# Kernel optimization log

Hardware: AMD Instinct MI355X
Metric: run time of the kernel (lower is better)

Reference implementation:

```python
import jax, jax.numpy as jnp
import numpy as np

B, S, T = 4, 4096, 2048
SD, TD, H = 512, 768, 8
D = SD // H
EPS = 1e-5
ALPHA_MAX = 0.5


def layer_norm(x, g, b):
    mu = jnp.mean(x, axis=-1, keepdims=True)
    var = jnp.mean(jnp.square(x - mu), axis=-1, keepdims=True)
    return (x - mu) * jax.lax.rsqrt(var + EPS) * g + b


def setup_inputs() -> dict:
    key = jax.random.key(0)
    ks = jax.random.split(key, 12)
    inp = {
        "source": jax.random.normal(ks[0], (B, S, SD), jnp.float32),
        "target": jax.random.normal(ks[1], (B, T, TD), jnp.float32),
        "target_mask": jax.random.randint(ks[2], (B, T), 0, 2, jnp.int32),
        # layer norms
        "ns_g": jnp.ones((SD,), jnp.float32), "ns_b": jnp.zeros((SD,), jnp.float32),
        "nt_g": jnp.ones((TD,), jnp.float32), "nt_b": jnp.zeros((TD,), jnp.float32),
        "no_g": jnp.ones((SD,), jnp.float32), "no_b": jnp.zeros((SD,), jnp.float32),
        # projections, stored (in, out); xavier-uniform with gains as in _init_weights
        "Wq": jax.random.uniform(ks[3], (SD, SD), jnp.float32, -1, 1) * (0.5 * np.sqrt(6.0 / (SD + SD))),
        "bq": jnp.zeros((SD,), jnp.float32),
        "Wk": jax.random.uniform(ks[4], (TD, SD), jnp.float32, -1, 1) * (0.5 * np.sqrt(6.0 / (TD + SD))),
        "bk": jnp.zeros((SD,), jnp.float32),
        "Wv": jax.random.uniform(ks[5], (TD, SD), jnp.float32, -1, 1) * (0.5 * np.sqrt(6.0 / (TD + SD))),
        "bv": jnp.zeros((SD,), jnp.float32),
        "Wo": jax.random.uniform(ks[6], (SD, SD), jnp.float32, -1, 1) * (0.25 * np.sqrt(6.0 / (SD + SD))),
        "bo": jnp.zeros((SD,), jnp.float32),
        "alpha_raw": jnp.asarray(0.1, jnp.float32),
    }
    return inp


def reference(source, target, target_mask, ns_g, ns_b, nt_g, nt_b, no_g, no_b,
              Wq, bq, Wk, bk, Wv, bv, Wo, bo, alpha_raw):
    scale = D ** -0.5
    src_n = layer_norm(source, ns_g, ns_b)
    tgt_n = layer_norm(target, nt_g, nt_b)
    Q = (src_n @ Wq + bq).reshape(B, S, H, D)
    K = (tgt_n @ Wk + bk).reshape(B, T, H, D)
    V = (tgt_n @ Wv + bv).reshape(B, T, H, D)
    attn = jnp.einsum('bshd,bthd->bhst', Q, K) * scale
    attn = jnp.clip(attn, -50.0, 50.0)
    mask = (target_mask == 0)[:, None, None, :]  # (B,1,1,T)
    attn = jnp.where(mask, -jnp.inf, attn)
    attn = jax.nn.softmax(attn, axis=-1)
    attn = jnp.nan_to_num(attn, nan=0.0)
    out = jnp.einsum('bhst,bthd->bshd', attn, V).reshape(B, S, SD)
    out = out @ Wo + bo
    out = layer_norm(out, no_g, no_b)
    alpha = ALPHA_MAX * (jnp.tanh(alpha_raw) + 1.0) / 2.0
    return source + alpha * out
```

## Files before the change

### kernel.cpp

```cpp
#include <hip/hip_runtime.h>
#include <math.h>

#define BB 4
#define SS 4096
#define TT 2048
#define SDIM 512
#define TDIM 768
#define NH 8
#define HD 64

typedef __attribute__((ext_vector_type(8))) short s8v;
typedef __attribute__((ext_vector_type(4))) short s4v;
typedef __attribute__((ext_vector_type(4))) float f32x4;
typedef __attribute__((ext_vector_type(4))) unsigned int u32x4;

__device__ inline unsigned short f2bf(float f) {
    unsigned int u = __float_as_uint(f);
    u += 0x7FFFu + ((u >> 16) & 1u);
    return (unsigned short)(u >> 16);
}

__device__ inline unsigned int cvtpk_bf16(float lo, float hi) {
    unsigned int r;
    asm("v_cvt_pk_bf16_f32 %0, %1, %2" : "=v"(r) : "v"(lo), "v"(hi));
    return r;
}

__global__ __launch_bounds__(256) void prep_w(const float* __restrict__ W,
                                              unsigned short* __restrict__ Wt,
                                              int K, int N, float scale) {
    __shared__ float tile[32][33];
    const int n0 = blockIdx.x * 32, k0 = blockIdx.y * 32;
    const int tx = threadIdx.x & 31, ty = threadIdx.x >> 5;
#pragma unroll
    for (int i = 0; i < 4; ++i) {
        const int k = ty + i * 8;
        tile[k][tx] = W[(size_t)(k0 + k) * N + n0 + tx];
    }
    __syncthreads();
#pragma unroll
    for (int i = 0; i < 4; ++i) {
        const int n = ty + i * 8;
        Wt[(size_t)(n0 + n) * K + k0 + tx] = f2bf(tile[tx][n] * scale);
    }
}

template <int W, int BLK>
__global__ __launch_bounds__(BLK) void ln_rows_bf(const float* __restrict__ x,
                                                  const float* __restrict__ g,
                                                  const float* __restrict__ bb,
                                                  unsigned short* __restrict__ y) {
    const int row = blockIdx.x;
    const int t = threadIdx.x;
    float4 v = *(const float4*)(x + (size_t)row * W + t * 4);
    float s = v.x + v.y + v.z + v.w;
    float q = v.x * v.x + v.y * v.y + v.z * v.z + v.w * v.w;
#pragma unroll
    for (int off = 32; off > 0; off >>= 1) {
        s += __shfl_down(s, off, 64);
        q += __shfl_down(q, off, 64);
    }
    constexpr int NW = BLK / 64;
    __shared__ float redS[NW], redQ[NW];
    if ((t & 63) == 0) { redS[t >> 6] = s; redQ[t >> 6] = q; }
    __syncthreads();
    float S = 0.f, Q = 0.f;
#pragma unroll
    for (int i = 0; i < NW; ++i) { S += redS[i]; Q += redQ[i]; }
    const float mu = S * (1.0f / W);
    const float var = Q * (1.0f / W) - mu * mu;
    const float rstd = rsqrtf(var + 1e-5f);
    const float4 gv = *(const float4*)(g + t * 4);
    const float4 bv = *(const float4*)(bb + t * 4);
    s4v o;
    o[0] = (short)f2bf((v.x - mu) * rstd * gv.x + bv.x);
    o[1] = (short)f2bf((v.y - mu) * rstd * gv.y + bv.y);
    o[2] = (short)f2bf((v.z - mu) * rstd * gv.z + bv.z);
    o[3] = (short)f2bf((v.w - mu) * rstd * gv.w + bv.w);
    *(s4v*)(y + (size_t)row * W + t * 4) = o;
}

__global__ __launch_bounds__(128) void ln_res(const float* __restrict__ x,
                                              const float* __restrict__ src,
                                              const float* __restrict__ g,
                                              const float* __restrict__ bb,
                                              const float* __restrict__ alpha_raw,
                                              float* __restrict__ out) {
    const int W = 512;
    const int row = blockIdx.x;
    const int t = threadIdx.x;
    float4 v = *(const float4*)(x + (size_t)row * W + t * 4);
    float s = v.x + v.y + v.z + v.w;
    float q = v.x * v.x + v.y * v.y + v.z * v.z + v.w * v.w;
#pragma unroll
    for (int off = 32; off > 0; off >>= 1) {
        s += __shfl_down(s, off, 64);
        q += __shfl_down(q, off, 64);
    }
    __shared__ float redS[2], redQ[2];
    if ((t & 63) == 0) { redS[t >> 6] = s; redQ[t >> 6] = q; }
    __syncthreads();
    const float S = redS[0] + redS[1];
    const float Q = redQ[0] + redQ[1];
    const float mu = S * (1.0f / W);
    const float var = Q * (1.0f / W) - mu * mu;
    const float rstd = rsqrtf(var + 1e-5f);
    const float alpha = 0.25f * (tanhf(alpha_raw[0]) + 1.0f);
    const float4 gv = *(const float4*)(g + t * 4);
    const float4 bv = *(const float4*)(bb + t * 4);
    const float4 sv = *(const float4*)(src + (size_t)row * W + t * 4);
    float4 o;
    o.x = sv.x + alpha * ((v.x - mu) * rstd * gv.x + bv.x);
    o.y = sv.y + alpha * ((v.y - mu) * rstd * gv.y + bv.y);
    o.z = sv.z + alpha * ((v.z - mu) * rstd * gv.z + bv.z);
    o.w = sv.w + alpha * ((v.w - mu) * rstd * gv.w + bv.w);
    *(float4*)(out + (size_t)row * W + t * 4) = o;
}

template <int OUT>
__global__ __launch_bounds__(256) void gemm_mfma(const unsigned short* __restrict__ A,
                                                 const unsigned short* __restrict__ Bt,
                                                 const float* __restrict__ bias,
                                                 void* __restrict__ C,
                                                 int N, int K, float bscale) {
    __shared__ __align__(16) char A_lds[128 * 128];
    __shared__ __align__(16) char B_lds[128 * 128];
    const int tid = threadIdx.x;
    const int l = tid & 63;
    const int lq = l & 15, q = l >> 4;
    const int w = tid >> 6;
    const int wr = w >> 1, wc = w & 1;
    const int m0 = blockIdx.y * 128, n0 = blockIdx.x * 128;

    f32x4 acc[4][4];
#pragma unroll
    for (int i = 0; i < 4; ++i)
#pragma unroll
        for (int j = 0; j < 4; ++j) acc[i][j] = (f32x4){0.f, 0.f, 0.f, 0.f};

    const int sr = tid >> 1;
    const int sc = (tid & 1) * 64;
    const int swz = (sr & 7) << 4;

    for (int k0 = 0; k0 < K; k0 += 64) {
        const unsigned short* ap = A + (size_t)(m0 + sr) * K + k0 + (sc >> 1);
        const unsigned short* bp = Bt + (size_t)(n0 + sr) * K + k0 + (sc >> 1);
#pragma unroll
        for (int c = 0; c < 4; ++c) {
            const s8v av = *(const s8v*)(ap + c * 8);
            *(s8v*)(A_lds + sr * 128 + ((sc + c * 16) ^ swz)) = av;
        }
#pragma unroll
        for (int c = 0; c < 4; ++c) {
            const s8v bv = *(const s8v*)(bp + c * 8);
            *(s8v*)(B_lds + sr * 128 + ((sc + c * 16) ^ swz)) = bv;
        }
        __syncthreads();
#pragma unroll
        for (int db = 0; db < 2; ++db) {
            s8v af[4], bf[4];
#pragma unroll
            for (int i = 0; i < 4; ++i) {
                const int ra = wr * 64 + i * 16 + lq;
                af[i] = *(const s8v*)(A_lds + ra * 128 + ((db * 64 + q * 16) ^ ((ra & 7) << 4)));
                const int rb = wc * 64 + i * 16 + lq;
                bf[i] = *(const s8v*)(B_lds + rb * 128 + ((db * 64 + q * 16) ^ ((rb & 7) << 4)));
            }
#pragma unroll
            for (int i = 0; i < 4; ++i)
#pragma unroll
                for (int j = 0; j < 4; ++j)
                    acc[i][j] = __builtin_amdgcn_mfma_f32_16x16x32_bf16(af[i], bf[j], acc[i][j], 0, 0, 0);
        }
        __syncthreads();
    }
#pragma unroll
    for (int i = 0; i < 4; ++i) {
#pragma unroll
        for (int j = 0; j < 4; ++j) {
            const int col = n0 + wc * 64 + j * 16 + lq;
            const float bs = bias[col] * bscale;
            const int mr0 = m0 + wr * 64 + i * 16 + q * 4;
            if (OUT == 0) {
                unsigned short* Cp = (unsigned short*)C;
#pragma unroll
                for (int r = 0; r < 4; ++r)
                    Cp[(size_t)(mr0 + r) * N + col] = f2bf(acc[i][j][r] + bs);
            } else if (OUT == 1) {
                float* Cp = (float*)C;
#pragma unroll
                for (int r = 0; r < 4; ++r)
                    Cp[(size_t)(mr0 + r) * N + col] = acc[i][j][r] + bs;
            } else {
                s4v o4;
#pragma unroll
                for (int r = 0; r < 4; ++r) o4[r] = (short)f2bf(acc[i][j][r] + bs);
                unsigned short* Cp = (unsigned short*)C;
                *(s4v*)(Cp + ((size_t)((mr0 >> 11) * SDIM + col)) * TT + (mr0 & 2047)) = o4;
            }
        }
    }
}

__global__ __launch_bounds__(256) void attn_mfma(const unsigned short* __restrict__ Qg,
                                                 const unsigned short* __restrict__ Kg,
                                                 const unsigned short* __restrict__ Vt,
                                                 const int* __restrict__ mask,
                                                 unsigned short* __restrict__ O) {
    __shared__ __align__(16) char K_lds[64 * 128];
    __shared__ __align__(16) char V_lds[64 * 128];
    __shared__ __align__(16) float Msb[64];
    const int b = blockIdx.y >> 3, h = blockIdx.y & 7;
    const int tid = threadIdx.x;
    const int w = tid >> 6, l = tid & 63;
    const int lq = l & 15, q = l >> 4;
    const int qrow = blockIdx.x * 64 + w * 16 + lq;

    s8v qf[2];
    {
        const unsigned short* qp = Qg + ((size_t)b * SS + qrow) * SDIM + h * HD + q * 8;
        qf[0] = *(const s8v*)(qp);
        qf[1] = *(const s8v*)(qp + 32);
    }
    f32x4 accO[4];
#pragma unroll
    for (int i = 0; i < 4; ++i) accO[i] = (f32x4){0.f, 0.f, 0.f, 0.f};
    float lsum = 0.f;

    const int sr = tid >> 2;
    const int sc = (tid & 3) * 32;
    const int swz = (sr & 7) << 4;

    for (int t0 = 0; t0 < TT; t0 += 64) {
        {
            const unsigned short* kp = Kg + ((size_t)b * TT + t0 + sr) * SDIM + h * HD + (sc >> 1);
            const s8v k0 = *(const s8v*)kp;
            const s8v k1 = *(const s8v*)(kp + 8);
            *(s8v*)(K_lds + sr * 128 + (sc ^ swz)) = k0;
            *(s8v*)(K_lds + sr * 128 + ((sc + 16) ^ swz)) = k1;
            const unsigned short* vp = Vt + ((size_t)(b * SDIM + h * HD + sr)) * TT + t0 + (sc >> 1);
            const s8v v0 = *(const s8v*)vp;
            const s8v v1 = *(const s8v*)(vp + 8);
            *(s8v*)(V_lds + sr * 128 + (sc ^ swz)) = v0;
            *(s8v*)(V_lds + sr * 128 + ((sc + 16) ^ swz)) = v1;
            if (tid < 64) Msb[tid] = (mask[b * TT + t0 + tid] == 0) ? -1e30f : 0.f;
        }
        __syncthreads();

        f32x4 accS[4];
#pragma unroll
        for (int kt = 0; kt < 4; ++kt) accS[kt] = *(const f32x4*)(Msb + kt * 16 + q * 4);
#pragma unroll
        for (int kt = 0; kt < 4; ++kt) {
            const int row = kt * 16 + lq;
            const int rs = (row & 7) << 4;
#pragma unroll
            for (int db = 0; db < 2; ++db) {
                const s8v af = *(const s8v*)(K_lds + row * 128 + ((db * 64 + q * 16) ^ rs));
                accS[kt] = __builtin_amdgcn_mfma_f32_16x16x32_bf16(af, qf[db], accS[kt], 0, 0, 0);
            }
        }
        float p[4][4];
#pragma unroll
        for (int kt = 0; kt < 4; ++kt) {
#pragma unroll
            for (int r = 0; r < 4; ++r) {
                const float pv = __expf(accS[kt][r]);
                p[kt][r] = pv;
                lsum += pv;
            }
        }
#pragma unroll
        for (int kb = 0; kb < 2; ++kb) {
            const int a = kb * 2;
            u32x4 pw;
            pw[0] = cvtpk_bf16(p[a][0], p[a][1]);
            pw[1] = cvtpk_bf16(p[a][2], p[a][3]);
            pw[2] = cvtpk_bf16(p[a + 1][0], p[a + 1][1]);
            pw[3] = cvtpk_bf16(p[a + 1][2], p[a + 1][3]);
            const s8v pb = __builtin_bit_cast(s8v, pw);
#pragma unroll
            for (int nt = 0; nt < 4; ++nt) {
                const int row = nt * 16 + lq;
                const int rs = (row & 7) << 4;
                const s4v lo = *(const s4v*)(V_lds + row * 128 + ((kb * 64 + q * 8) ^ rs));
                const s4v hi = *(const s4v*)(V_lds + row * 128 + ((kb * 64 + 32 + q * 8) ^ rs));
                const s8v vf = __builtin_shufflevector(lo, hi, 0, 1, 2, 3, 4, 5, 6, 7);
                accO[nt] = __builtin_amdgcn_mfma_f32_16x16x32_bf16(vf, pb, accO[nt], 0, 0, 0);
            }
        }
        __syncthreads();
    }
    lsum += __shfl_xor(lsum, 16, 64);
    lsum += __shfl_xor(lsum, 32, 64);
    const float inv = (lsum > 0.f) ? 1.0f / lsum : 0.f;
    unsigned short* op = O + ((size_t)b * SS + qrow) * SDIM + h * HD + q * 4;
#pragma unroll
    for (int nt = 0; nt < 4; ++nt) {
        s4v o4;
#pragma unroll
        for (int r = 0; r < 4; ++r) o4[r] = (short)f2bf(accO[nt][r] * inv);
        *(s4v*)(op + nt * 16) = o4;
    }
}

extern "C" void kernel_launch(void* const* d_in, const int* in_sizes, int n_in,
                              void* d_out, int out_size, void* d_ws, size_t ws_size,
                              hipStream_t stream) {
    const float* src = (const float*)d_in[0];
    const float* tgt = (const float*)d_in[1];
    const int* tmask = (const int*)d_in[2];
    const float* ns_g = (const float*)d_in[3];
    const float* ns_b = (const float*)d_in[4];
    const float* nt_g = (const float*)d_in[5];
    const float* nt_b = (const float*)d_in[6];
    const float* no_g = (const float*)d_in[7];
    const float* no_b = (const float*)d_in[8];
    const float* Wq = (const float*)d_in[9];
    const float* bq = (const float*)d_in[10];
    const float* Wk = (const float*)d_in[11];
    const float* bk = (const float*)d_in[12];
    const float* Wv = (const float*)d_in[13];
    const float* bv = (const float*)d_in[14];
    const float* Wo = (const float*)d_in[15];
    const float* bo = (const float*)d_in[16];
    const float* alpha_raw = (const float*)d_in[17];

    char* ws = (char*)d_ws;
    unsigned short* src_n = (unsigned short*)ws; ws += (size_t)16384 * 512 * 2;
    unsigned short* tgt_n = (unsigned short*)ws; ws += (size_t)8192 * 768 * 2;
    unsigned short* Qb    = (unsigned short*)ws; ws += (size_t)16384 * 512 * 2;
    unsigned short* Kb    = (unsigned short*)ws; ws += (size_t)8192 * 512 * 2;
    unsigned short* Vtb   = (unsigned short*)ws; ws += (size_t)8192 * 512 * 2;
    unsigned short* Oa    = (unsigned short*)ws; ws += (size_t)16384 * 512 * 2;
    float*          Opj   = (float*)ws;          ws += (size_t)16384 * 512 * 4;
    unsigned short* Wtq   = (unsigned short*)ws; ws += (size_t)512 * 512 * 2;
    unsigned short* Wtk   = (unsigned short*)ws; ws += (size_t)512 * 768 * 2;
    unsigned short* Wtv   = (unsigned short*)ws; ws += (size_t)512 * 768 * 2;
    unsigned short* Wto   = (unsigned short*)ws; ws += (size_t)512 * 512 * 2;

    prep_w<<<dim3(16, 16), 256, 0, stream>>>(Wq, Wtq, 512, 512, 0.125f);
    prep_w<<<dim3(16, 24), 256, 0, stream>>>(Wk, Wtk, 768, 512, 1.0f);
    prep_w<<<dim3(16, 24), 256, 0, stream>>>(Wv, Wtv, 768, 512, 1.0f);
    prep_w<<<dim3(16, 16), 256, 0, stream>>>(Wo, Wto, 512, 512, 1.0f);

    ln_rows_bf<512, 128><<<16384, 128, 0, stream>>>(src, ns_g, ns_b, src_n);
    ln_rows_bf<768, 192><<<8192, 192, 0, stream>>>(tgt, nt_g, nt_b, tgt_n);

    gemm_mfma<0><<<dim3(4, 128), 256, 0, stream>>>(src_n, Wtq, bq, Qb, 512, 512, 0.125f);
    gemm_mfma<0><<<dim3(4, 64), 256, 0, stream>>>(tgt_n, Wtk, bk, Kb, 512, 768, 1.0f);
    gemm_mfma<2><<<dim3(4, 64), 256, 0, stream>>>(tgt_n, Wtv, bv, Vtb, 512, 768, 1.0f);

    attn_mfma<<<dim3(64, 32), 256, 0, stream>>>(Qb, Kb, Vtb, tmask, Oa);

    gemm_mfma<1><<<dim3(4, 128), 256, 0, stream>>>(Oa, Wto, bo, Opj, 512, 512, 1.0f);

    ln_res<<<16384, 128, 0, stream>>>(Opj, src, no_g, no_b, alpha_raw, (float*)d_out);
}
```

Measured before the change: 368.0 us.

## Double-buffer attention K/V tiles, widen query block, shrink GEMM N-tile, merge weight prep

The attention kernel now double-buffers K, V and mask tiles in LDS, prefetching the next tile into registers while computing the current one. Each wave handles two 16-row query groups so every K/V fragment read from LDS feeds two MFMAs, and MFMA sections are bracketed with s_setprio. The projection GEMMs use a 128x64 tile instead of 128x128, doubling grid size for better CU occupancy and wave count. The four weight-prep launches are merged into one 3D-grid launch. Costs are doubled LDS for attention, extra registers for the prefetch and the second query group, and more B-tile reloads in the GEMMs.

```diff
diff --git a/kernel.cpp b/kernel.cpp
--- a/kernel.cpp
+++ b/kernel.cpp
@@ -26,11 +26,24 @@
     return r;
 }
 
-__global__ __launch_bounds__(256) void prep_w(const float* __restrict__ W,
-                                              unsigned short* __restrict__ Wt,
-                                              int K, int N, float scale) {
+__global__ __launch_bounds__(256) void prep_w4(const float* __restrict__ W0,
+                                               const float* __restrict__ W1,
+                                               const float* __restrict__ W2,
+                                               const float* __restrict__ W3,
+                                               unsigned short* __restrict__ T0,
+                                               unsigned short* __restrict__ T1,
+                                               unsigned short* __restrict__ T2,
+                                               unsigned short* __restrict__ T3) {
+    const int z = blockIdx.z;
+    const int K = (z == 1 || z == 2) ? 768 : 512;
+    const int k0 = blockIdx.y * 32;
+    if (k0 >= K) return;
+    const float* W = (z == 0) ? W0 : (z == 1) ? W1 : (z == 2) ? W2 : W3;
+    unsigned short* Wt = (z == 0) ? T0 : (z == 1) ? T1 : (z == 2) ? T2 : T3;
+    const float scale = (z == 0) ? 0.125f : 1.0f;
+    const int N = 512;
     __shared__ float tile[32][33];
-    const int n0 = blockIdx.x * 32, k0 = blockIdx.y * 32;
+    const int n0 = blockIdx.x * 32;
     const int tx = threadIdx.x & 31, ty = threadIdx.x >> 5;
 #pragma unroll
     for (int i = 0; i < 4; ++i) {
@@ -124,52 +137,58 @@
                                                  void* __restrict__ C,
                                                  int N, int K, float bscale) {
     __shared__ __align__(16) char A_lds[128 * 128];
-    __shared__ __align__(16) char B_lds[128 * 128];
+    __shared__ __align__(16) char B_lds[64 * 128];
     const int tid = threadIdx.x;
     const int l = tid & 63;
     const int lq = l & 15, q = l >> 4;
     const int w = tid >> 6;
     const int wr = w >> 1, wc = w & 1;
-    const int m0 = blockIdx.y * 128, n0 = blockIdx.x * 128;
-
-    f32x4 acc[4][4];
+    const int m0 = blockIdx.y * 128, n0 = blockIdx.x * 64;
+
+    f32x4 acc[4][2];
 #pragma unroll
     for (int i = 0; i < 4; ++i)
 #pragma unroll
-        for (int j = 0; j < 4; ++j) acc[i][j] = (f32x4){0.f, 0.f, 0.f, 0.f};
+        for (int j = 0; j < 2; ++j) acc[i][j] = (f32x4){0.f, 0.f, 0.f, 0.f};
 
     const int sr = tid >> 1;
     const int sc = (tid & 1) * 64;
-    const int swz = (sr & 7) << 4;
+    const int swzA = (sr & 7) << 4;
+    const int sr2 = tid >> 2;
+    const int sc2 = (tid & 3) * 32;
+    const int swzB = (sr2 & 7) << 4;
 
     for (int k0 = 0; k0 < K; k0 += 64) {
         const unsigned short* ap = A + (size_t)(m0 + sr) * K + k0 + (sc >> 1);
-        const unsigned short* bp = Bt + (size_t)(n0 + sr) * K + k0 + (sc >> 1);
+        const unsigned short* bp = Bt + (size_t)(n0 + sr2) * K + k0 + (sc2 >> 1);
 #pragma unroll
         for (int c = 0; c < 4; ++c) {
             const s8v av = *(const s8v*)(ap + c * 8);
-            *(s8v*)(A_lds + sr * 128 + ((sc + c * 16) ^ swz)) = av;
-        }
-#pragma unroll
-        for (int c = 0; c < 4; ++c) {
+            *(s8v*)(A_lds + sr * 128 + ((sc + c * 16) ^ swzA)) = av;
+        }
+#pragma unroll
+        for (int c = 0; c < 2; ++c) {
             const s8v bv = *(const s8v*)(bp + c * 8);
-            *(s8v*)(B_lds + sr * 128 + ((sc + c * 16) ^ swz)) = bv;
+            *(s8v*)(B_lds + sr2 * 128 + ((sc2 + c * 16) ^ swzB)) = bv;
         }
         __syncthreads();
 #pragma unroll
         for (int db = 0; db < 2; ++db) {
-            s8v af[4], bf[4];
+            s8v af[4], bf[2];
 #pragma unroll
             for (int i = 0; i < 4; ++i) {
                 const int ra = wr * 64 + i * 16 + lq;
                 af[i] = *(const s8v*)(A_lds + ra * 128 + ((db * 64 + q * 16) ^ ((ra & 7) << 4)));
-                const int rb = wc * 64 + i * 16 + lq;
-                bf[i] = *(const s8v*)(B_lds + rb * 128 + ((db * 64 + q * 16) ^ ((rb & 7) << 4)));
+            }
+#pragma unroll
+            for (int j = 0; j < 2; ++j) {
+                const int rb = wc * 32 + j * 16 + lq;
+                bf[j] = *(const s8v*)(B_lds + rb * 128 + ((db * 64 + q * 16) ^ ((rb & 7) << 4)));
             }
 #pragma unroll
             for (int i = 0; i < 4; ++i)
 #pragma unroll
-                for (int j = 0; j < 4; ++j)
+                for (int j = 0; j < 2; ++j)
                     acc[i][j] = __builtin_amdgcn_mfma_f32_16x16x32_bf16(af[i], bf[j], acc[i][j], 0, 0, 0);
         }
         __syncthreads();
@@ -177,8 +196,8 @@
 #pragma unroll
     for (int i = 0; i < 4; ++i) {
 #pragma unroll
-        for (int j = 0; j < 4; ++j) {
-            const int col = n0 + wc * 64 + j * 16 + lq;
+        for (int j = 0; j < 2; ++j) {
+            const int col = n0 + wc * 32 + j * 16 + lq;
             const float bs = bias[col] * bscale;
             const int mr0 = m0 + wr * 64 + i * 16 + q * 4;
             if (OUT == 0) {
@@ -207,100 +226,136 @@
                                                  const unsigned short* __restrict__ Vt,
                                                  const int* __restrict__ mask,
                                                  unsigned short* __restrict__ O) {
-    __shared__ __align__(16) char K_lds[64 * 128];
-    __shared__ __align__(16) char V_lds[64 * 128];
-    __shared__ __align__(16) float Msb[64];
+    __shared__ __align__(16) char K_lds[2][64 * 128];
+    __shared__ __align__(16) char V_lds[2][64 * 128];
+    __shared__ __align__(16) float Msb[2][64];
     const int b = blockIdx.y >> 3, h = blockIdx.y & 7;
     const int tid = threadIdx.x;
     const int w = tid >> 6, l = tid & 63;
     const int lq = l & 15, q = l >> 4;
-    const int qrow = blockIdx.x * 64 + w * 16 + lq;
-
-    s8v qf[2];
+    const int qbase = blockIdx.x * 128 + w * 32;
+
+    s8v qf[2][2];
+#pragma unroll
+    for (int qa = 0; qa < 2; ++qa) {
+        const unsigned short* qp = Qg + ((size_t)b * SS + qbase + qa * 16 + lq) * SDIM + h * HD + q * 8;
+        qf[qa][0] = *(const s8v*)(qp);
+        qf[qa][1] = *(const s8v*)(qp + 32);
+    }
+    f32x4 accO[2][4];
+#pragma unroll
+    for (int qa = 0; qa < 2; ++qa)
+#pragma unroll
+        for (int nt = 0; nt < 4; ++nt) accO[qa][nt] = (f32x4){0.f, 0.f, 0.f, 0.f};
+    float lsum[2] = {0.f, 0.f};
+
+    const int sr = tid >> 2;
+    const int scb = (tid & 3) * 32;
+    const int swz = (sr & 7) << 4;
+    const unsigned short* kp_base = Kg + ((size_t)b * TT + sr) * SDIM + h * HD + (scb >> 1);
+    const unsigned short* vp_base = Vt + ((size_t)(b * SDIM + h * HD + sr)) * TT + (scb >> 1);
+
     {
-        const unsigned short* qp = Qg + ((size_t)b * SS + qrow) * SDIM + h * HD + q * 8;
-        qf[0] = *(const s8v*)(qp);
-        qf[1] = *(const s8v*)(qp + 32);
-    }
-    f32x4 accO[4];
-#pragma unroll
-    for (int i = 0; i < 4; ++i) accO[i] = (f32x4){0.f, 0.f, 0.f, 0.f};
-    float lsum = 0.f;
-
-    const int sr = tid >> 2;
-    const int sc = (tid & 3) * 32;
-    const int swz = (sr & 7) << 4;
+        const s8v k0r = *(const s8v*)kp_base;
+        const s8v k1r = *(const s8v*)(kp_base + 8);
+        const s8v v0r = *(const s8v*)vp_base;
+        const s8v v1r = *(const s8v*)(vp_base + 8);
+        *(s8v*)(K_lds[0] + sr * 128 + (scb ^ swz)) = k0r;
+        *(s8v*)(K_lds[0] + sr * 128 + ((scb + 16) ^ swz)) = k1r;
+        *(s8v*)(V_lds[0] + sr * 128 + (scb ^ swz)) = v0r;
+        *(s8v*)(V_lds[0] + sr * 128 + ((scb + 16) ^ swz)) = v1r;
+        if (tid < 64) Msb[0][tid] = (mask[b * TT + tid] == 0) ? -1e30f : 0.f;
+    }
+    __syncthreads();
 
     for (int t0 = 0; t0 < TT; t0 += 64) {
-        {
-            const unsigned short* kp = Kg + ((size_t)b * TT + t0 + sr) * SDIM + h * HD + (sc >> 1);
-            const s8v k0 = *(const s8v*)kp;
-            const s8v k1 = *(const s8v*)(kp + 8);
-            *(s8v*)(K_lds + sr * 128 + (sc ^ swz)) = k0;
-            *(s8v*)(K_lds + sr * 128 + ((sc + 16) ^ swz)) = k1;
-            const unsigned short* vp = Vt + ((size_t)(b * SDIM + h * HD + sr)) * TT + t0 + (sc >> 1);
-            const s8v v0 = *(const s8v*)vp;
-            const s8v v1 = *(const s8v*)(vp + 8);
-            *(s8v*)(V_lds + sr * 128 + (sc ^ swz)) = v0;
-            *(s8v*)(V_lds + sr * 128 + ((sc + 16) ^ swz)) = v1;
-            if (tid < 64) Msb[tid] = (mask[b * TT + t0 + tid] == 0) ? -1e30f : 0.f;
-        }
-        __syncthreads();
-
-        f32x4 accS[4];
-#pragma unroll
-        for (int kt = 0; kt < 4; ++kt) accS[kt] = *(const f32x4*)(Msb + kt * 16 + q * 4);
+        const int cur = (t0 >> 6) & 1, nxt = cur ^ 1;
+        const bool has_next = (t0 + 64) < TT;
+
+        s8v kn0, kn1, vn0, vn1;
+        int mn = 0;
+        if (has_next) {
+            const unsigned short* kp = kp_base + (size_t)(t0 + 64) * SDIM;
+            const unsigned short* vp = vp_base + (t0 + 64);
+            kn0 = *(const s8v*)kp;
+            kn1 = *(const s8v*)(kp + 8);
+            vn0 = *(const s8v*)vp;
+            vn1 = *(const s8v*)(vp + 8);
+            if (tid < 64) mn = mask[b * TT + t0 + 64 + tid];
+        }
+
+        u32x4 pb[2][2];
 #pragma unroll
         for (int kt = 0; kt < 4; ++kt) {
             const int row = kt * 16 + lq;
             const int rs = (row & 7) << 4;
+            const f32x4 mb = *(const f32x4*)(&Msb[cur][kt * 16 + q * 4]);
+            f32x4 aS0 = mb, aS1 = mb;
+            __builtin_amdgcn_s_setprio(1);
 #pragma unroll
             for (int db = 0; db < 2; ++db) {
-                const s8v af = *(const s8v*)(K_lds + row * 128 + ((db * 64 + q * 16) ^ rs));
-                accS[kt] = __builtin_amdgcn_mfma_f32_16x16x32_bf16(af, qf[db], accS[kt], 0, 0, 0);
-            }
-        }
-        float p[4][4];
-#pragma unroll
-        for (int kt = 0; kt < 4; ++kt) {
-#pragma unroll
-            for (int r = 0; r < 4; ++r) {
-                const float pv = __expf(accS[kt][r]);
-                p[kt][r] = pv;
-                lsum += pv;
+                const s8v af = *(const s8v*)(K_lds[cur] + row * 128 + ((db * 64 + q * 16) ^ rs));
+                aS0 = __builtin_amdgcn_mfma_f32_16x16x32_bf16(af, qf[0][db], aS0, 0, 0, 0);
+                aS1 = __builtin_amdgcn_mfma_f32_16x16x32_bf16(af, qf[1][db], aS1, 0, 0, 0);
+            }
+            __builtin_amdgcn_s_setprio(0);
+            {
+                const float p0 = __expf(aS0[0]), p1 = __expf(aS0[1]);
+                const float p2 = __expf(aS0[2]), p3 = __expf(aS0[3]);
+                lsum[0] += (p0 + p1) + (p2 + p3);
+                pb[kt >> 1][0][(kt & 1) * 2 + 0] = cvtpk_bf16(p0, p1);
+                pb[kt >> 1][0][(kt & 1) * 2 + 1] = cvtpk_bf16(p2, p3);
+            }
+            {
+                const float p0 = __expf(aS1[0]), p1 = __expf(aS1[1]);
+                const float p2 = __expf(aS1[2]), p3 = __expf(aS1[3]);
+                lsum[1] += (p0 + p1) + (p2 + p3);
+                pb[kt >> 1][1][(kt & 1) * 2 + 0] = cvtpk_bf16(p0, p1);
+                pb[kt >> 1][1][(kt & 1) * 2 + 1] = cvtpk_bf16(p2, p3);
             }
         }
 #pragma unroll
         for (int kb = 0; kb < 2; ++kb) {
-            const int a = kb * 2;
-            u32x4 pw;
-            pw[0] = cvtpk_bf16(p[a][0], p[a][1]);
-            pw[1] = cvtpk_bf16(p[a][2], p[a][3]);
-            pw[2] = cvtpk_bf16(p[a + 1][0], p[a + 1][1]);
-            pw[3] = cvtpk_bf16(p[a + 1][2], p[a + 1][3]);
-            const s8v pb = __builtin_bit_cast(s8v, pw);
+            const s8v pb0 = __builtin_bit_cast(s8v, pb[kb][0]);
+            const s8v pb1 = __builtin_bit_cast(s8v, pb[kb][1]);
+            __builtin_amdgcn_s_setprio(1);
 #pragma unroll
             for (int nt = 0; nt < 4; ++nt) {
                 const int row = nt * 16 + lq;
                 const int rs = (row & 7) << 4;
-                const s4v lo = *(const s4v*)(V_lds + row * 128 + ((kb * 64 + q * 8) ^ rs));
-                const s4v hi = *(const s4v*)(V_lds + row * 128 + ((kb * 64 + 32 + q * 8) ^ rs));
+                const s4v lo = *(const s4v*)(V_lds[cur] + row * 128 + ((kb * 64 + q * 8) ^ rs));
+                const s4v hi = *(const s4v*)(V_lds[cur] + row * 128 + ((kb * 64 + 32 + q * 8) ^ rs));
                 const s8v vf = __builtin_shufflevector(lo, hi, 0, 1, 2, 3, 4, 5, 6, 7);
-                accO[nt] = __builtin_amdgcn_mfma_f32_16x16x32_bf16(vf, pb, accO[nt], 0, 0, 0);
-            }
+                accO[0][nt] = __builtin_amdgcn_mfma_f32_16x16x32_bf16(vf, pb0, accO[0][nt], 0, 0, 0);
+                accO[1][nt] = __builtin_amdgcn_mfma_f32_16x16x32_bf16(vf, pb1, accO[1][nt], 0, 0, 0);
+            }
+            __builtin_amdgcn_s_setprio(0);
+        }
+
+        if (has_next) {
+            *(s8v*)(K_lds[nxt] + sr * 128 + (scb ^ swz)) = kn0;
+            *(s8v*)(K_lds[nxt] + sr * 128 + ((scb + 16) ^ swz)) = kn1;
+            *(s8v*)(V_lds[nxt] + sr * 128 + (scb ^ swz)) = vn0;
+            *(s8v*)(V_lds[nxt] + sr * 128 + ((scb + 16) ^ swz)) = vn1;
+            if (tid < 64) Msb[nxt][tid] = (mn == 0) ? -1e30f : 0.f;
         }
         __syncthreads();
     }
-    lsum += __shfl_xor(lsum, 16, 64);
-    lsum += __shfl_xor(lsum, 32, 64);
-    const float inv = (lsum > 0.f) ? 1.0f / lsum : 0.f;
-    unsigned short* op = O + ((size_t)b * SS + qrow) * SDIM + h * HD + q * 4;
-#pragma unroll
-    for (int nt = 0; nt < 4; ++nt) {
-        s4v o4;
-#pragma unroll
-        for (int r = 0; r < 4; ++r) o4[r] = (short)f2bf(accO[nt][r] * inv);
-        *(s4v*)(op + nt * 16) = o4;
+
+#pragma unroll
+    for (int qa = 0; qa < 2; ++qa) {
+        float ls = lsum[qa];
+        ls += __shfl_xor(ls, 16, 64);
+        ls += __shfl_xor(ls, 32, 64);
+        const float inv = (ls > 0.f) ? 1.0f / ls : 0.f;
+        unsigned short* op = O + ((size_t)b * SS + qbase + qa * 16 + lq) * SDIM + h * HD + q * 4;
+#pragma unroll
+        for (int nt = 0; nt < 4; ++nt) {
+            s4v o4;
+#pragma unroll
+            for (int r = 0; r < 4; ++r) o4[r] = (short)f2bf(accO[qa][nt][r] * inv);
+            *(s4v*)(op + nt * 16) = o4;
+        }
     }
 }
 
@@ -339,21 +394,18 @@
     unsigned short* Wtv   = (unsigned short*)ws; ws += (size_t)512 * 768 * 2;
     unsigned short* Wto   = (unsigned short*)ws; ws += (size_t)512 * 512 * 2;
 
-    prep_w<<<dim3(16, 16), 256, 0, stream>>>(Wq, Wtq, 512, 512, 0.125f);
-    prep_w<<<dim3(16, 24), 256, 0, stream>>>(Wk, Wtk, 768, 512, 1.0f);
-    prep_w<<<dim3(16, 24), 256, 0, stream>>>(Wv, Wtv, 768, 512, 1.0f);
-    prep_w<<<dim3(16, 16), 256, 0, stream>>>(Wo, Wto, 512, 512, 1.0f);
+    prep_w4<<<dim3(16, 24, 4), 256, 0, stream>>>(Wq, Wk, Wv, Wo, Wtq, Wtk, Wtv, Wto);
 
     ln_rows_bf<512, 128><<<16384, 128, 0, stream>>>(src, ns_g, ns_b, src_n);
     ln_rows_bf<768, 192><<<8192, 192, 0, stream>>>(tgt, nt_g, nt_b, tgt_n);
 
-    gemm_mfma<0><<<dim3(4, 128), 256, 0, stream>>>(src_n, Wtq, bq, Qb, 512, 512, 0.125f);
-    gemm_mfma<0><<<dim3(4, 64), 256, 0, stream>>>(tgt_n, Wtk, bk, Kb, 512, 768, 1.0f);
-    gemm_mfma<2><<<dim3(4, 64), 256, 0, stream>>>(tgt_n, Wtv, bv, Vtb, 512, 768, 1.0f);
-
-    attn_mfma<<<dim3(64, 32), 256, 0, stream>>>(Qb, Kb, Vtb, tmask, Oa);
-
-    gemm_mfma<1><<<dim3(4, 128), 256, 0, stream>>>(Oa, Wto, bo, Opj, 512, 512, 1.0f);
+    gemm_mfma<0><<<dim3(8, 128), 256, 0, stream>>>(src_n, Wtq, bq, Qb, 512, 512, 0.125f);
+    gemm_mfma<0><<<dim3(8, 64), 256, 0, stream>>>(tgt_n, Wtk, bk, Kb, 512, 768, 1.0f);
+    gemm_mfma<2><<<dim3(8, 64), 256, 0, stream>>>(tgt_n, Wtv, bv, Vtb, 512, 768, 1.0f);
+
+    attn_mfma<<<dim3(32, 32), 256, 0, stream>>>(Qb, Kb, Vtb, tmask, Oa);
+
+    gemm_mfma<1><<<dim3(8, 128), 256, 0, stream>>>(Oa, Wto, bo, Opj, 512, 512, 1.0f);
 
     ln_res<<<16384, 128, 0, stream>>>(Opj, src, no_g, no_b, alpha_raw, (float*)d_out);
 }
```

Result: faster. 349.5 us (-5.0%).
